# Optimization experiments

Hardware: AMD Instinct MI355X
Metric: run time of the kernel (lower is better)

Reference implementation:

```python
import jax, jax.numpy as jnp
import numpy as np

K = 1024  # init kwarg k


def setup_inputs() -> dict:
    key = jax.random.key(0)
    k1, k2 = jax.random.split(key)
    B, N, F = 8, 50000, 256
    node_embs = jax.random.normal(k1, (B, N, F), dtype=jnp.float32)
    mask = jnp.zeros((B, N), dtype=jnp.float32)  # additive mask (0 = keep)
    stdv = 1.0 / np.sqrt(F)
    scorer = jax.random.uniform(k2, (F, 1), dtype=jnp.float32, minval=-stdv, maxval=stdv)
    return {"node_embs": node_embs, "mask": mask, "scorer": scorer}


def reference(node_embs, mask, scorer):
    # scores: [B, N] = node_embs @ scorer / ||scorer||, plus additive mask
    scores = jnp.einsum('bnf,f->bn', node_embs, scorer[:, 0]) / jnp.linalg.norm(scorer)
    scores = scores + mask
    # top-k over node dim
    vals, topk_idx = jax.lax.top_k(scores, K)  # [B, K]
    # gather selected node embeddings and scale by tanh of their scores
    gathered = jnp.take_along_axis(node_embs, topk_idx[:, :, None], axis=1)  # [B, K, F]
    gate = jnp.tanh(jnp.take_along_axis(scores, topk_idx, axis=1))  # [B, K]
    out = gathered * gate[:, :, None]
    return out.transpose(0, 2, 1)  # [B, F, K]
```

## Files before the change

### kernel.cpp

```cpp
#include <hip/hip_runtime.h>
#include <math.h>

#define BB 8
#define NN 50000
#define FF 256
#define KK 1024

__device__ __forceinline__ unsigned long long key64(double x) {
    unsigned long long u = (unsigned long long)__double_as_longlong(x);
    u ^= (u & 0x8000000000000000ull) ? 0xFFFFFFFFFFFFFFFFull : 0x8000000000000000ull;
    return u;
}

__global__ __launch_bounds__(256) void score_kernel(const float* __restrict__ emb,
                                                    const float* __restrict__ mask,
                                                    const float* __restrict__ scorer,
                                                    double* __restrict__ scores) {
    const int lane = threadIdx.x & 63;
    const int wave = threadIdx.x >> 6;

    float4 sc = ((const float4*)scorer)[lane];

    double n2 = (double)sc.x * sc.x + (double)sc.y * sc.y +
                (double)sc.z * sc.z + (double)sc.w * sc.w;
    #pragma unroll
    for (int off = 32; off; off >>= 1) n2 += __shfl_xor(n2, off, 64);
    const double inv_norm = 1.0 / sqrt(n2);

    const long rows = (long)BB * NN;
    const long wid  = (long)blockIdx.x * 4 + wave;
    const long nw   = (long)gridDim.x * 4;

    for (long r = wid; r < rows; r += nw) {
        float4 v = ((const float4*)emb)[r * 64 + lane];
        double d = (double)v.x * sc.x + (double)v.y * sc.y +
                   (double)v.z * sc.z + (double)v.w * sc.w;
        #pragma unroll
        for (int off = 32; off; off >>= 1) d += __shfl_xor(d, off, 64);
        if (lane == 0) scores[r] = d * inv_norm + (double)mask[r];
    }
}

__global__ __launch_bounds__(1024) void select_kernel(const double* __restrict__ scores,
                                                      int* __restrict__ topk_idx,
                                                      float* __restrict__ gate) {
    const int b   = blockIdx.x;
    const int tid = threadIdx.x;
    const double* sc = scores + (long)b * NN;

    __shared__ unsigned int hist[2048];
    __shared__ unsigned long long prefix_sh;
    __shared__ int need_sh;
    __shared__ unsigned int cand_count;
    __shared__ unsigned long long keyA[4096];
    __shared__ int idxA[4096];

    if (tid == 0) { prefix_sh = 0ull; need_sh = KK; cand_count = 0u; }
    __syncthreads();

    const int shifts[2] = {53, 42};

    for (int p = 0; p < 2; p++) {
        for (int i = tid; i < 2048; i += 1024) hist[i] = 0u;
        __syncthreads();
        const unsigned long long pref = prefix_sh;
        const int sh = shifts[p];
        for (int i = tid * 2; i < NN; i += 2048) {
            double2 v = *(const double2*)(sc + i);
            unsigned long long k0 = key64(v.x);
            unsigned long long k1 = key64(v.y);
            if (p == 0 || (k0 >> 53) == pref) atomicAdd(&hist[(unsigned)((k0 >> sh) & 2047ull)], 1u);
            if (p == 0 || (k1 >> 53) == pref) atomicAdd(&hist[(unsigned)((k1 >> sh) & 2047ull)], 1u);
        }
        __syncthreads();
        if (tid == 0) {
            unsigned int cum = 0; int need = need_sh; int selbin = 0; unsigned int above = 0;
            for (int bin = 2047; bin >= 0; bin--) {
                unsigned int c = hist[bin];
                if (cum + c >= (unsigned int)need) { selbin = bin; above = cum; break; }
                cum += c;
            }
            prefix_sh = (prefix_sh << 11) | (unsigned long long)selbin;
            need_sh = need - (int)above;
        }
        __syncthreads();
    }

    const unsigned long long pfx = prefix_sh;
    for (int i = tid * 2; i < NN; i += 2048) {
        double2 v = *(const double2*)(sc + i);
        unsigned long long k0 = key64(v.x);
        unsigned long long k1 = key64(v.y);
        if ((k0 >> 42) >= pfx) {
            unsigned int pos = atomicAdd(&cand_count, 1u);
            if (pos < 4096u) { keyA[pos] = k0; idxA[pos] = i; }
        }
        if ((k1 >> 42) >= pfx) {
            unsigned int pos = atomicAdd(&cand_count, 1u);
            if (pos < 4096u) { keyA[pos] = k1; idxA[pos] = i + 1; }
        }
    }
    __syncthreads();
    const unsigned int M = cand_count < 4096u ? cand_count : 4096u;
    for (int i = (int)M + tid; i < 4096; i += 1024) { keyA[i] = 0ull; idxA[i] = 0x7fffffff; }
    __syncthreads();

    for (int kk = 2; kk <= 4096; kk <<= 1) {
        for (int j = kk >> 1; j > 0; j >>= 1) {
            for (int i = tid; i < 4096; i += 1024) {
                int partner = i ^ j;
                if (partner > i) {
                    unsigned long long ka = keyA[i], kb = keyA[partner];
                    int ia = idxA[i], ib = idxA[partner];
                    bool a_before_b = (ka > kb) || (ka == kb && ia < ib);
                    bool b_before_a = (kb > ka) || (kb == ka && ib < ia);
                    bool descBlock = ((i & kk) == 0);
                    bool doSwap = descBlock ? b_before_a : a_before_b;
                    if (doSwap) {
                        keyA[i] = kb; keyA[partner] = ka;
                        idxA[i] = ib; idxA[partner] = ia;
                    }
                }
            }
            __syncthreads();
        }
    }

    for (int i = tid; i < KK; i += 1024) {
        int idx = idxA[i];
        topk_idx[b * KK + i] = idx;
        gate[b * KK + i] = tanhf((float)sc[idx]);
    }
}

__global__ __launch_bounds__(256) void gather_kernel(const float* __restrict__ emb,
                                                     const int* __restrict__ topk_idx,
                                                     const float* __restrict__ gate,
                                                     float* __restrict__ out) {
    const int b  = blockIdx.x >> 5;
    const int kt = blockIdx.x & 31;
    const int k0 = kt * 32;
    const int tid = threadIdx.x;

    __shared__ float tile[32][FF + 4];
    __shared__ int   s_idx[32];
    __shared__ float s_gate[32];

    if (tid < 32) {
        s_idx[tid]  = topk_idx[b * KK + k0 + tid];
        s_gate[tid] = gate[b * KK + k0 + tid];
    }
    __syncthreads();

    const int g = tid >> 6, lane = tid & 63;
    #pragma unroll
    for (int i = 0; i < 8; i++) {
        int kl = i * 4 + g;
        int row = s_idx[kl];
        float gt = s_gate[kl];
        float4 v = ((const float4*)(emb + ((long)b * NN + row) * FF))[lane];
        float* t = &tile[kl][lane * 4];
        t[0] = v.x * gt; t[1] = v.y * gt; t[2] = v.z * gt; t[3] = v.w * gt;
    }
    __syncthreads();

    const long outbase = ((long)b * FF) * KK + k0;
    #pragma unroll
    for (int c = 0; c < 32; c++) {
        int linear = c * 256 + tid;
        int f = linear >> 5;
        int k = linear & 31;
        out[outbase + (long)f * KK + k] = tile[k][f];
    }
}

extern "C" void kernel_launch(void* const* d_in, const int* in_sizes, int n_in,
                              void* d_out, int out_size, void* d_ws, size_t ws_size,
                              hipStream_t stream) {
    const float* emb    = (const float*)d_in[0];
    const float* mask   = (const float*)d_in[1];
    const float* scorer = (const float*)d_in[2];
    float* out = (float*)d_out;

    char* wsb = (char*)d_ws;
    double* scores  = (double*)wsb;
    int*    topkidx = (int*)(wsb + sizeof(double) * BB * NN);
    float*  gate    = (float*)(wsb + sizeof(double) * BB * NN
                                   + sizeof(int) * BB * KK);

    score_kernel<<<2048, 256, 0, stream>>>(emb, mask, scorer, scores);
    select_kernel<<<BB, 1024, 0, stream>>>(scores, topkidx, gate);
    gather_kernel<<<BB * 32, 256, 0, stream>>>(emb, topkidx, gate, out);
}
```

Before: 755.4 us.

## Fuse first radix histogram into scoring and replace bitonic sort with rank counting

Measured after the change: 719.7 us. 4.7% less time.

```diff
diff --git a/kernel.cpp b/kernel.cpp
--- a/kernel.cpp
+++ b/kernel.cpp
@@ -5,131 +5,172 @@
 #define NN 50000
 #define FF 256
 #define KK 1024
+#define CHUNK 400
+#define NCHUNK 125
 
 __device__ __forceinline__ unsigned long long key64(double x) {
     unsigned long long u = (unsigned long long)__double_as_longlong(x);
     u ^= (u & 0x8000000000000000ull) ? 0xFFFFFFFFFFFFFFFFull : 0x8000000000000000ull;
     return u;
 }
+__device__ __forceinline__ double key_to_double(unsigned long long k) {
+    unsigned long long u = (k & 0x8000000000000000ull) ? (k ^ 0x8000000000000000ull) : ~k;
+    return __longlong_as_double((long long)u);
+}
+
+__global__ __launch_bounds__(1024) void zero_kernel(unsigned int* __restrict__ p, int n) {
+    int i = blockIdx.x * 1024 + threadIdx.x;
+    if (i < n) p[i] = 0u;
+}
 
 __global__ __launch_bounds__(256) void score_kernel(const float* __restrict__ emb,
                                                     const float* __restrict__ mask,
                                                     const float* __restrict__ scorer,
-                                                    double* __restrict__ scores) {
+                                                    double* __restrict__ scores,
+                                                    unsigned int* __restrict__ ghist) {
+    const int b    = blockIdx.x / NCHUNK;
+    const int c    = blockIdx.x % NCHUNK;
+    const int n0   = c * CHUNK;
     const int lane = threadIdx.x & 63;
     const int wave = threadIdx.x >> 6;
 
+    __shared__ unsigned int h[2048];
+    __shared__ float smask[CHUNK];
+    for (int i = threadIdx.x; i < 2048; i += 256) h[i] = 0u;
+    for (int i = threadIdx.x; i < CHUNK; i += 256) smask[i] = mask[b * NN + n0 + i];
+    __syncthreads();
+
     float4 sc = ((const float4*)scorer)[lane];
-
     double n2 = (double)sc.x * sc.x + (double)sc.y * sc.y +
                 (double)sc.z * sc.z + (double)sc.w * sc.w;
     #pragma unroll
     for (int off = 32; off; off >>= 1) n2 += __shfl_xor(n2, off, 64);
     const double inv_norm = 1.0 / sqrt(n2);
 
-    const long rows = (long)BB * NN;
-    const long wid  = (long)blockIdx.x * 4 + wave;
-    const long nw   = (long)gridDim.x * 4;
-
-    for (long r = wid; r < rows; r += nw) {
-        float4 v = ((const float4*)emb)[r * 64 + lane];
-        double d = (double)v.x * sc.x + (double)v.y * sc.y +
+    const float* base  = emb + ((long)b * NN + n0) * FF;
+    double*      sbase = scores + (long)b * NN + n0;
+
+    for (int it = 0; it < CHUNK / 16; ++it) {
+        const int nn = it * 16 + wave * 4;
+        double d[4];
+        #pragma unroll
+        for (int j = 0; j < 4; j++) {
+            float4 v = ((const float4*)(base + (nn + j) * FF))[lane];
+            d[j] = (double)v.x * sc.x + (double)v.y * sc.y +
                    (double)v.z * sc.z + (double)v.w * sc.w;
+        }
         #pragma unroll
-        for (int off = 32; off; off >>= 1) d += __shfl_xor(d, off, 64);
-        if (lane == 0) scores[r] = d * inv_norm + (double)mask[r];
+        for (int off = 32; off; off >>= 1) {
+            #pragma unroll
+            for (int j = 0; j < 4; j++) d[j] += __shfl_xor(d[j], off, 64);
+        }
+        if (lane == 0) {
+            double s[4];
+            #pragma unroll
+            for (int j = 0; j < 4; j++) {
+                s[j] = d[j] * inv_norm + (double)smask[nn + j];
+                atomicAdd(&h[(unsigned)(key64(s[j]) >> 53)], 1u);
+            }
+            *(double2*)(sbase + nn)     = make_double2(s[0], s[1]);
+            *(double2*)(sbase + nn + 2) = make_double2(s[2], s[3]);
+        }
+    }
+    __syncthreads();
+
+    unsigned int* gh = ghist + b * 2048;
+    for (int i = threadIdx.x; i < 2048; i += 256) {
+        unsigned int v = h[i];
+        if (v) atomicAdd(&gh[i], v);
     }
 }
 
 __global__ __launch_bounds__(1024) void select_kernel(const double* __restrict__ scores,
+                                                      const unsigned int* __restrict__ ghist,
                                                       int* __restrict__ topk_idx,
                                                       float* __restrict__ gate) {
     const int b   = blockIdx.x;
     const int tid = threadIdx.x;
     const double* sc = scores + (long)b * NN;
 
-    __shared__ unsigned int hist[2048];
-    __shared__ unsigned long long prefix_sh;
-    __shared__ int need_sh;
-    __shared__ unsigned int cand_count;
+    __shared__ unsigned int h[2048];
     __shared__ unsigned long long keyA[4096];
     __shared__ int idxA[4096];
-
-    if (tid == 0) { prefix_sh = 0ull; need_sh = KK; cand_count = 0u; }
-    __syncthreads();
-
-    const int shifts[2] = {53, 42};
-
-    for (int p = 0; p < 2; p++) {
-        for (int i = tid; i < 2048; i += 1024) hist[i] = 0u;
-        __syncthreads();
-        const unsigned long long pref = prefix_sh;
-        const int sh = shifts[p];
-        for (int i = tid * 2; i < NN; i += 2048) {
-            double2 v = *(const double2*)(sc + i);
-            unsigned long long k0 = key64(v.x);
-            unsigned long long k1 = key64(v.y);
-            if (p == 0 || (k0 >> 53) == pref) atomicAdd(&hist[(unsigned)((k0 >> sh) & 2047ull)], 1u);
-            if (p == 0 || (k1 >> 53) == pref) atomicAdd(&hist[(unsigned)((k1 >> sh) & 2047ull)], 1u);
-        }
-        __syncthreads();
-        if (tid == 0) {
-            unsigned int cum = 0; int need = need_sh; int selbin = 0; unsigned int above = 0;
-            for (int bin = 2047; bin >= 0; bin--) {
-                unsigned int c = hist[bin];
-                if (cum + c >= (unsigned int)need) { selbin = bin; above = cum; break; }
-                cum += c;
-            }
-            prefix_sh = (prefix_sh << 11) | (unsigned long long)selbin;
-            need_sh = need - (int)above;
-        }
-        __syncthreads();
-    }
-
-    const unsigned long long pfx = prefix_sh;
-    for (int i = tid * 2; i < NN; i += 2048) {
-        double2 v = *(const double2*)(sc + i);
-        unsigned long long k0 = key64(v.x);
-        unsigned long long k1 = key64(v.y);
+    __shared__ int bin1_s, need2_s, bin2_s;
+    __shared__ unsigned int cnt;
+
+    const int i0 = tid, i1 = tid + 1024;
+
+    h[i0] = ghist[b * 2048 + i0];
+    h[i1] = ghist[b * 2048 + i1];
+    if (tid == 0) cnt = 0u;
+    __syncthreads();
+
+    for (int off = 1; off < 2048; off <<= 1) {
+        unsigned a0 = (i0 + off < 2048) ? h[i0 + off] : 0u;
+        unsigned a1 = (i1 + off < 2048) ? h[i1 + off] : 0u;
+        __syncthreads();
+        h[i0] += a0; h[i1] += a1;
+        __syncthreads();
+    }
+    if (h[i0] >= (unsigned)KK && (i0 == 2047 || h[i0 + 1] < (unsigned)KK)) {
+        bin1_s = i0; need2_s = KK - (int)((i0 == 2047) ? 0u : h[i0 + 1]);
+    }
+    if (h[i1] >= (unsigned)KK && (i1 == 2047 || h[i1 + 1] < (unsigned)KK)) {
+        bin1_s = i1; need2_s = KK - (int)((i1 == 2047) ? 0u : h[i1 + 1]);
+    }
+    __syncthreads();
+    const unsigned long long bin1 = (unsigned long long)bin1_s;
+    const unsigned need2 = (unsigned)need2_s;
+
+    h[i0] = 0u; h[i1] = 0u;
+    __syncthreads();
+    for (int i = tid; i < NN / 2; i += 1024) {
+        double2 v = ((const double2*)sc)[i];
+        unsigned long long k0 = key64(v.x), k1 = key64(v.y);
+        if ((k0 >> 53) == bin1) atomicAdd(&h[(unsigned)((k0 >> 42) & 2047ull)], 1u);
+        if ((k1 >> 53) == bin1) atomicAdd(&h[(unsigned)((k1 >> 42) & 2047ull)], 1u);
+    }
+    __syncthreads();
+
+    for (int off = 1; off < 2048; off <<= 1) {
+        unsigned a0 = (i0 + off < 2048) ? h[i0 + off] : 0u;
+        unsigned a1 = (i1 + off < 2048) ? h[i1 + off] : 0u;
+        __syncthreads();
+        h[i0] += a0; h[i1] += a1;
+        __syncthreads();
+    }
+    if (h[i0] >= need2 && (i0 == 2047 || h[i0 + 1] < need2)) bin2_s = i0;
+    if (h[i1] >= need2 && (i1 == 2047 || h[i1 + 1] < need2)) bin2_s = i1;
+    __syncthreads();
+    const unsigned long long pfx = (bin1 << 11) | (unsigned long long)bin2_s;
+
+    for (int i = tid; i < NN / 2; i += 1024) {
+        double2 v = ((const double2*)sc)[i];
+        unsigned long long k0 = key64(v.x), k1 = key64(v.y);
         if ((k0 >> 42) >= pfx) {
-            unsigned int pos = atomicAdd(&cand_count, 1u);
-            if (pos < 4096u) { keyA[pos] = k0; idxA[pos] = i; }
+            unsigned p = atomicAdd(&cnt, 1u);
+            if (p < 4096u) { keyA[p] = k0; idxA[p] = 2 * i; }
         }
         if ((k1 >> 42) >= pfx) {
-            unsigned int pos = atomicAdd(&cand_count, 1u);
-            if (pos < 4096u) { keyA[pos] = k1; idxA[pos] = i + 1; }
-        }
-    }
-    __syncthreads();
-    const unsigned int M = cand_count < 4096u ? cand_count : 4096u;
-    for (int i = (int)M + tid; i < 4096; i += 1024) { keyA[i] = 0ull; idxA[i] = 0x7fffffff; }
-    __syncthreads();
-
-    for (int kk = 2; kk <= 4096; kk <<= 1) {
-        for (int j = kk >> 1; j > 0; j >>= 1) {
-            for (int i = tid; i < 4096; i += 1024) {
-                int partner = i ^ j;
-                if (partner > i) {
-                    unsigned long long ka = keyA[i], kb = keyA[partner];
-                    int ia = idxA[i], ib = idxA[partner];
-                    bool a_before_b = (ka > kb) || (ka == kb && ia < ib);
-                    bool b_before_a = (kb > ka) || (kb == ka && ib < ia);
-                    bool descBlock = ((i & kk) == 0);
-                    bool doSwap = descBlock ? b_before_a : a_before_b;
-                    if (doSwap) {
-                        keyA[i] = kb; keyA[partner] = ka;
-                        idxA[i] = ib; idxA[partner] = ia;
-                    }
-                }
-            }
-            __syncthreads();
-        }
-    }
-
-    for (int i = tid; i < KK; i += 1024) {
-        int idx = idxA[i];
-        topk_idx[b * KK + i] = idx;
-        gate[b * KK + i] = tanhf((float)sc[idx]);
+            unsigned p = atomicAdd(&cnt, 1u);
+            if (p < 4096u) { keyA[p] = k1; idxA[p] = 2 * i + 1; }
+        }
+    }
+    __syncthreads();
+    const int M = (int)(cnt < 4096u ? cnt : 4096u);
+
+    for (int i = tid; i < M; i += 1024) {
+        const unsigned long long ki = keyA[i];
+        const int ii = idxA[i];
+        int rank = 0;
+        for (int j = 0; j < M; ++j) {
+            const unsigned long long kj = keyA[j];
+            rank += (kj > ki) || (kj == ki && idxA[j] < ii);
+        }
+        if (rank < KK) {
+            topk_idx[b * KK + rank] = ii;
+            gate[b * KK + rank]     = tanhf((float)key_to_double(ki));
+        }
     }
 }
 
@@ -183,12 +224,13 @@
     float* out = (float*)d_out;
 
     char* wsb = (char*)d_ws;
-    double* scores  = (double*)wsb;
-    int*    topkidx = (int*)(wsb + sizeof(double) * BB * NN);
-    float*  gate    = (float*)(wsb + sizeof(double) * BB * NN
-                                   + sizeof(int) * BB * KK);
-
-    score_kernel<<<2048, 256, 0, stream>>>(emb, mask, scorer, scores);
-    select_kernel<<<BB, 1024, 0, stream>>>(scores, topkidx, gate);
-    gather_kernel<<<BB * 32, 256, 0, stream>>>(emb, topkidx, gate, out);
-}
+    double*       scores  = (double*)wsb;
+    unsigned int* ghist   = (unsigned int*)(wsb + sizeof(double) * BB * NN);
+    int*          topkidx = (int*)((char*)ghist + sizeof(unsigned int) * BB * 2048);
+    float*        gatep   = (float*)((char*)topkidx + sizeof(int) * BB * KK);
+
+    zero_kernel<<<16, 1024, 0, stream>>>(ghist, BB * 2048);
+    score_kernel<<<BB * NCHUNK, 256, 0, stream>>>(emb, mask, scorer, scores, ghist);
+    select_kernel<<<BB, 1024, 0, stream>>>(scores, ghist, topkidx, gatep);
+    gather_kernel<<<BB * 32, 256, 0, stream>>>(emb, topkidx, gatep, out);
+}
```
